# Kernel tuning notes

Hardware: AMD Instinct MI355X
Metric: run time of the kernel (lower is better)

## Reference

```python
import jax, jax.numpy as jnp
import numpy as np

DIM = 192
HEADS = 6
WS = (4, 8, 8)  # window size (D, H, W)
N = WS[0] * WS[1] * WS[2]  # 256 tokens per window
NW = 64
B_ = 256  # batch * nW


def _relative_position_index(ws):
    d, h, w = ws
    coords = jnp.stack(jnp.meshgrid(jnp.arange(d), jnp.arange(h), jnp.arange(w), indexing='ij'))
    coords = coords.reshape(3, -1)  # (3, N)
    rel = coords[:, :, None] - coords[:, None, :]  # (3, N, N)
    rel = rel.transpose(1, 2, 0) + jnp.array([d - 1, h - 1, w - 1])
    idx = rel[..., 0] * ((2 * h - 1) * (2 * w - 1)) + rel[..., 1] * (2 * w - 1) + rel[..., 2]
    return idx.astype(jnp.int32)  # (N, N)


def setup_inputs() -> dict:
    key = jax.random.key(0)
    ks = jax.random.split(key, 7)
    table_rows = (2 * WS[0] - 1) * (2 * WS[1] - 1) * (2 * WS[2] - 1)  # 1575
    return {
        'x': jax.random.normal(ks[0], (B_, N, DIM), dtype=jnp.float32),
        'mask': jax.random.normal(ks[1], (NW, N, N), dtype=jnp.float32),
        'qkv_w': jax.random.normal(ks[2], (DIM, 3 * DIM), dtype=jnp.float32) * 0.02,
        'qkv_b': jnp.zeros((3 * DIM,), dtype=jnp.float32),
        'proj_w': jax.random.normal(ks[3], (DIM, DIM), dtype=jnp.float32) * 0.02,
        'proj_b': jnp.zeros((DIM,), dtype=jnp.float32),
        'bias_table': jax.random.normal(ks[4], (table_rows, HEADS), dtype=jnp.float32) * 0.02,
        'rel_index': _relative_position_index(WS),
    }


def reference(x, mask, qkv_w, qkv_b, proj_w, proj_b, bias_table, rel_index):
    B, Ntok, C = x.shape
    hd = C // HEADS
    scale = hd ** (-0.5)
    qkv = (x @ qkv_w + qkv_b).reshape(B, Ntok, 3, HEADS, hd)
    qkv = qkv.transpose(2, 0, 3, 1, 4)  # (3, B, H, N, hd)
    q, k, v = qkv[0], qkv[1], qkv[2]
    attn = jnp.einsum('bhnd,bhmd->bhnm', q * scale, k)  # (B, H, N, N)
    # gathered relative-position bias: (N, N, H) -> (H, N, N)
    bias = bias_table[rel_index.reshape(-1)].reshape(Ntok, Ntok, HEADS).transpose(2, 0, 1)
    attn = attn + bias[None]
    nW = mask.shape[0]
    attn = attn.reshape(B // nW, nW, HEADS, Ntok, Ntok) + mask[None, :, None]
    attn = attn.reshape(B, HEADS, Ntok, Ntok)
    attn = jax.nn.softmax(attn, axis=-1)
    out = jnp.einsum('bhnm,bhmd->bhnd', attn, v)  # (B, H, N, hd)
    out = out.transpose(0, 2, 1, 3).reshape(B, Ntok, C)
    out = out @ proj_w + proj_b
    return out
```

## Files before the change

kernel.cpp:

```cpp
#include <hip/hip_runtime.h>
#include <cstdint>
#include <math.h>

#define DIMC 192
#define NTOK 256
#define HEADS 6
#define HD 32
#define L2E 1.4426950408889634f

typedef __bf16 bf16x8 __attribute__((ext_vector_type(8)));
typedef __bf16 bf16x4 __attribute__((ext_vector_type(4)));
typedef float f32x4 __attribute__((ext_vector_type(4)));

__device__ __forceinline__ void gload_lds16(const __bf16* g, __bf16* l) {
    __builtin_amdgcn_global_load_lds((const __attribute__((address_space(1))) void*)g,
                                     (__attribute__((address_space(3))) void*)l, 16, 0, 0);
}

__global__ void prep(const float* __restrict__ x, __bf16* __restrict__ xb,
                     const float* __restrict__ qkv_w, __bf16* __restrict__ wqt,
                     const float* __restrict__ proj_w, __bf16* __restrict__ wpt,
                     const float* __restrict__ table, const int* __restrict__ rel,
                     __bf16* __restrict__ biasb) {
    const int bid = blockIdx.x, t = threadIdx.x;
    if (bid < 6144) {
        int i = bid * 256 + t;
        float4 a = ((const float4*)x)[i * 2];
        float4 b = ((const float4*)x)[i * 2 + 1];
        bf16x8 o = {(__bf16)a.x, (__bf16)a.y, (__bf16)a.z, (__bf16)a.w,
                    (__bf16)b.x, (__bf16)b.y, (__bf16)b.z, (__bf16)b.w};
        ((bf16x8*)xb)[i] = o;
    } else if (bid < 6576) {
        int i = (bid - 6144) * 256 + t;
        int n = i / DIMC, k = i - n * DIMC;
        wqt[i] = (__bf16)qkv_w[(size_t)k * 576 + n];
    } else if (bid < 6720) {
        int i = (bid - 6576) * 256 + t;
        int n = i / DIMC, k = i - n * DIMC;
        wpt[i] = (__bf16)proj_w[(size_t)k * DIMC + n];
    } else {
        int i = (bid - 6720) * 256 + t;
        int h = i >> 16;
        int r = i & 65535;
        biasb[i] = (__bf16)(table[rel[r] * 6 + h] * L2E);
    }
}

__launch_bounds__(256, 2)
__global__ void qkvbm(const __bf16* __restrict__ A, const __bf16* __restrict__ Wt,
                      const float* __restrict__ bias,
                      __bf16* __restrict__ qo, __bf16* __restrict__ ko, __bf16* __restrict__ vo,
                      const float* __restrict__ mask, const __bf16* __restrict__ biasb,
                      __bf16* __restrict__ bm) {
    __shared__ __bf16 As[256 * 64];
    __shared__ __bf16 Bs[96 * 64];
    const int t = threadIdx.x;
    const int lin = blockIdx.x;

    if (lin >= 1536) {
        int i = (lin - 1536) * 256 + t;
        int w = i >> 13, oct = i & 8191;
        float4 m0 = ((const float4*)mask)[(size_t)w * 16384 + oct * 2];
        float4 m1 = ((const float4*)mask)[(size_t)w * 16384 + oct * 2 + 1];
        #pragma unroll
        for (int h = 0; h < 6; ++h) {
            bf16x8 bb = ((const bf16x8*)biasb)[h * 8192 + oct];
            bf16x8 o = {(__bf16)(m0.x * L2E + (float)bb[0]), (__bf16)(m0.y * L2E + (float)bb[1]),
                        (__bf16)(m0.z * L2E + (float)bb[2]), (__bf16)(m0.w * L2E + (float)bb[3]),
                        (__bf16)(m1.x * L2E + (float)bb[4]), (__bf16)(m1.y * L2E + (float)bb[5]),
                        (__bf16)(m1.z * L2E + (float)bb[6]), (__bf16)(m1.w * L2E + (float)bb[7])};
            ((bf16x8*)bm)[(size_t)(w * 6 + h) * 8192 + oct] = o;
        }
        return;
    }

    const int wv = t >> 6, lane = t & 63;
    const int l16 = lane & 15, quad = lane >> 4;
    const int xcd = lin & 7, pos = lin >> 3;
    const int bx = pos % 6;
    const int by = xcd + (pos / 6) * 8;
    const int m0 = by * 256;
    const int j0 = bx * 96;

    f32x4 acc[4][6];
    #pragma unroll
    for (int mt = 0; mt < 4; ++mt)
        #pragma unroll
        for (int nt = 0; nt < 6; ++nt)
            acc[mt][nt] = (f32x4){0.f, 0.f, 0.f, 0.f};

    for (int kit = 0; kit < 3; ++kit) {
        const int k0 = kit * 64;
        #pragma unroll
        for (int gi = 0; gi < 8; ++gi) {
            int g = wv * 8 + gi;
            int cid = g * 64 + lane;
            int row = cid >> 3, kcs = cid & 7;
            int kcg = kcs ^ (row & 7);
            gload_lds16(A + (size_t)(m0 + row) * DIMC + k0 + kcg * 8, As + g * 512);
        }
        #pragma unroll
        for (int gi = 0; gi < 3; ++gi) {
            int g = wv * 3 + gi;
            int cid = g * 64 + lane;
            int n = cid >> 3, kcs = cid & 7;
            int kcg = kcs ^ (n & 7);
            gload_lds16(Wt + (size_t)(j0 + n) * DIMC + k0 + kcg * 8, Bs + g * 512);
        }
        __syncthreads();
        #pragma unroll
        for (int kk = 0; kk < 2; ++kk) {
            bf16x8 af[4], bfr[6];
            #pragma unroll
            for (int mt = 0; mt < 4; ++mt) {
                int row = wv * 64 + mt * 16 + l16;
                int ch = (kk * 4 + quad) ^ (row & 7);
                af[mt] = *(const bf16x8*)(As + row * 64 + ch * 8);
            }
            #pragma unroll
            for (int nt = 0; nt < 6; ++nt) {
                int n = nt * 16 + l16;
                int ch = (kk * 4 + quad) ^ (n & 7);
                bfr[nt] = *(const bf16x8*)(Bs + n * 64 + ch * 8);
            }
            #pragma unroll
            for (int mt = 0; mt < 4; ++mt)
                #pragma unroll
                for (int nt = 0; nt < 6; ++nt)
                    acc[mt][nt] = __builtin_amdgcn_mfma_f32_16x16x32_bf16(af[mt], bfr[nt], acc[mt][nt], 0, 0, 0);
        }
        __syncthreads();
    }

    const int which = bx >> 1;
    __bf16* outp = which == 0 ? qo : (which == 1 ? ko : vo);
    const float sc = which == 0 ? (0.17677669529663687f * L2E) : 1.0f;
    float bq[6];
    #pragma unroll
    for (int nt = 0; nt < 6; ++nt) bq[nt] = bias[j0 + nt * 16 + l16];
    const int cloc = (bx & 1) * 96;
    const int b = m0 >> 8;

    if (which != 2) {
        __bf16* tile = As + wv * 4096;
        const int TP = 104;
        #pragma unroll
        for (int mt = 0; mt < 4; ++mt) {
            #pragma unroll
            for (int nt = 0; nt < 6; ++nt)
                #pragma unroll
                for (int r = 0; r < 4; ++r)
                    tile[(quad * 4 + r) * TP + nt * 16 + l16] = (__bf16)((acc[mt][nt][r] + bq[nt]) * sc);
            int row = lane >> 2;
            #pragma unroll
            for (int it = 0; it < 3; ++it) {
                int c8 = (lane & 3) + it * 4;
                bf16x8 val = *(const bf16x8*)(tile + row * TP + c8 * 8);
                int n = wv * 64 + mt * 16 + row;
                int cw = cloc + c8 * 8;
                int h = cw >> 5, d0 = cw & 31;
                *(bf16x8*)(outp + (((size_t)b * HEADS + h) * NTOK + n) * HD + d0) = val;
            }
        }
    } else {
        __bf16* tileT = As + wv * 4096;
        #pragma unroll
        for (int mt = 0; mt < 4; ++mt) {
            #pragma unroll
            for (int nt = 0; nt < 6; ++nt)
                #pragma unroll
                for (int r = 0; r < 4; ++r)
                    tileT[(nt * 16 + l16) * 16 + quad * 4 + r] = (__bf16)(acc[mt][nt][r] + bq[nt]);
            int n0 = wv * 64 + mt * 16;
            #pragma unroll
            for (int it = 0; it < 3; ++it) {
                int qid = lane + 64 * it;
                int col = qid >> 1, half = qid & 1;
                bf16x8 val = *(const bf16x8*)(tileT + col * 16 + half * 8);
                int cw = cloc + col;
                int h = cw >> 5, d = cw & 31;
                *(bf16x8*)(outp + (((size_t)b * HEADS + h) * HD + d) * NTOK + n0 + half * 8) = val;
            }
        }
    }
}

__launch_bounds__(256, 4)
__global__ void attn_mfma(const __bf16* __restrict__ qg, const __bf16* __restrict__ kg,
                          const __bf16* __restrict__ vtg, const __bf16* __restrict__ bm,
                          __bf16* __restrict__ aout) {
    __shared__ __bf16 Ks[NTOK * 32];
    __shared__ __bf16 VTs[HD * 256];
    __shared__ __bf16 Ps[4][16][40];

    const int lin = blockIdx.x;
    const int xcd = lin & 7, pos = lin >> 3;
    const int g = xcd + (pos >> 2) * 8;
    const int i4 = pos & 3;
    const int h = g % 6, w = g / 6;
    const int b = i4 * 64 + w;
    const int bh = b * HEADS + h;

    const int t = threadIdx.x;
    const int wv = t >> 6, lane = t & 63;
    const int l16 = lane & 15, quad = lane >> 4;
    const int q0 = wv * 64;
    const size_t base = (size_t)bh * (NTOK * HD);

    #pragma unroll
    for (int it = 0; it < 4; ++it) {
        int grp = it * 4 + wv;
        int cid = grp * 64 + lane;
        int row = cid >> 2, cc = cid & 3;
        int scc = cc ^ ((row >> 1) & 3);
        gload_lds16(kg + base + row * HD + scc * 8, Ks + grp * 512);
    }
    #pragma unroll
    for (int it = 0; it < 4; ++it) {
        int grp = it * 4 + wv;
        int cid = grp * 64 + lane;
        int row = cid >> 5, cc = cid & 31;
        int scc = cc ^ (row & 7);
        gload_lds16(vtg + base + row * NTOK + scc * 8, VTs + grp * 512);
    }
    __syncthreads();

    bf16x8 qf[4];
    #pragma unroll
    for (int qt = 0; qt < 4; ++qt)
        qf[qt] = *(const bf16x8*)(qg + base + (size_t)(q0 + qt * 16 + l16) * HD + quad * 8);

    f32x4 o[4][2];
    #pragma unroll
    for (int qt = 0; qt < 4; ++qt)
        #pragma unroll
        for (int dt = 0; dt < 2; ++dt)
            o[qt][dt] = (f32x4){0.f, 0.f, 0.f, 0.f};
    float rsum[4] = {};

    const __bf16* bmq = bm + (size_t)(w * 6 + h) * 65536 + (size_t)(q0 + l16) * 256 + quad * 4;
    const int ck = quad ^ ((l16 >> 1) & 3);
    const int xv = l16 & 7;

    bf16x4 bmv[4][2];
    #pragma unroll
    for (int qt = 0; qt < 4; ++qt)
        #pragma unroll
        for (int kt = 0; kt < 2; ++kt)
            bmv[qt][kt] = *(const bf16x4*)(bmq + qt * 4096 + kt * 16);

    for (int c = 0; c < 8; ++c) {
        const int kb = c * 32;
        bf16x4 bmn[4][2];
        if (c < 7) {
            #pragma unroll
            for (int qt = 0; qt < 4; ++qt)
                #pragma unroll
                for (int kt = 0; kt < 2; ++kt)
                    bmn[qt][kt] = *(const bf16x4*)(bmq + qt * 4096 + kb + 32 + kt * 16);
        }
        bf16x8 kf[2];
        #pragma unroll
        for (int kt = 0; kt < 2; ++kt)
            kf[kt] = *(const bf16x8*)(Ks + (kb + kt * 16 + l16) * 32 + ck * 8);
        bf16x8 vf[2];
        #pragma unroll
        for (int dt = 0; dt < 2; ++dt) {
            int cv = (c * 4 + quad) ^ xv;
            vf[dt] = *(const bf16x8*)(VTs + (dt * 16 + l16) * 256 + cv * 8);
        }

        #pragma unroll
        for (int qt = 0; qt < 4; ++qt) {
            #pragma unroll
            for (int kt = 0; kt < 2; ++kt) {
                f32x4 s = (f32x4){0.f, 0.f, 0.f, 0.f};
                s = __builtin_amdgcn_mfma_f32_16x16x32_bf16(kf[kt], qf[qt], s, 0, 0, 0);
                bf16x4 pk;
                #pragma unroll
                for (int r = 0; r < 4; ++r) {
                    float p = __builtin_amdgcn_exp2f(s[r] + (float)bmv[qt][kt][r]);
                    rsum[qt] += p;
                    pk[r] = (__bf16)p;
                }
                *(bf16x4*)(&Ps[wv][l16][kt * 16 + quad * 4]) = pk;
            }
            bf16x8 pf = *(const bf16x8*)(&Ps[wv][l16][quad * 8]);
            #pragma unroll
            for (int dt = 0; dt < 2; ++dt)
                o[qt][dt] = __builtin_amdgcn_mfma_f32_16x16x32_bf16(pf, vf[dt], o[qt][dt], 0, 0, 0);
        }
        if (c < 7) {
            #pragma unroll
            for (int qt = 0; qt < 4; ++qt)
                #pragma unroll
                for (int kt = 0; kt < 2; ++kt)
                    bmv[qt][kt] = bmn[qt][kt];
        }
    }

    float rstot[4];
    #pragma unroll
    for (int qt = 0; qt < 4; ++qt) {
        float s = rsum[qt];
        s += __shfl_xor(s, 16);
        s += __shfl_xor(s, 32);
        rstot[qt] = 1.0f / s;
    }
    #pragma unroll
    for (int qt = 0; qt < 4; ++qt) {
        #pragma unroll
        for (int r = 0; r < 4; ++r) {
            float inv = __shfl(rstot[qt], (lane & 48) | (quad * 4 + r));
            int qrow = q0 + qt * 16 + quad * 4 + r;
            #pragma unroll
            for (int dt = 0; dt < 2; ++dt)
                aout[((size_t)b * NTOK + qrow) * DIMC + h * HD + dt * 16 + l16] =
                    (__bf16)(o[qt][dt][r] * inv);
        }
    }
}

__launch_bounds__(256, 2)
__global__ void proj_mfma(const __bf16* __restrict__ A, const __bf16* __restrict__ Wt,
                          const float* __restrict__ bias, float* __restrict__ out) {
    __shared__ __bf16 As[256 * 64];
    __shared__ __bf16 Bs[96 * 64];
    const int t = threadIdx.x;
    const int wv = t >> 6, lane = t & 63;
    const int l16 = lane & 15, quad = lane >> 4;

    const int lin = blockIdx.x + blockIdx.y * 2;
    const int xcd = lin & 7, pos = lin >> 3;
    const int bx = pos & 1;
    const int by = xcd + (pos >> 1) * 8;

    const int m0 = by * 256;
    const int j0 = bx * 96;

    f32x4 acc[4][6];
    #pragma unroll
    for (int mt = 0; mt < 4; ++mt)
        #pragma unroll
        for (int nt = 0; nt < 6; ++nt)
            acc[mt][nt] = (f32x4){0.f, 0.f, 0.f, 0.f};

    for (int kit = 0; kit < 3; ++kit) {
        const int k0 = kit * 64;
        #pragma unroll
        for (int gi = 0; gi < 8; ++gi) {
            int g = wv * 8 + gi;
            int cid = g * 64 + lane;
            int row = cid >> 3, kcs = cid & 7;
            int kcg = kcs ^ (row & 7);
            gload_lds16(A + (size_t)(m0 + row) * DIMC + k0 + kcg * 8, As + g * 512);
        }
        #pragma unroll
        for (int gi = 0; gi < 3; ++gi) {
            int g = wv * 3 + gi;
            int cid = g * 64 + lane;
            int n = cid >> 3, kcs = cid & 7;
            int kcg = kcs ^ (n & 7);
            gload_lds16(Wt + (size_t)(j0 + n) * DIMC + k0 + kcg * 8, Bs + g * 512);
        }
        __syncthreads();
        #pragma unroll
        for (int kk = 0; kk < 2; ++kk) {
            bf16x8 af[4], bfr[6];
            #pragma unroll
            for (int mt = 0; mt < 4; ++mt) {
                int row = wv * 64 + mt * 16 + l16;
                int ch = (kk * 4 + quad) ^ (row & 7);
                af[mt] = *(const bf16x8*)(As + row * 64 + ch * 8);
            }
            #pragma unroll
            for (int nt = 0; nt < 6; ++nt) {
                int n = nt * 16 + l16;
                int ch = (kk * 4 + quad) ^ (n & 7);
                bfr[nt] = *(const bf16x8*)(Bs + n * 64 + ch * 8);
            }
            #pragma unroll
            for (int mt = 0; mt < 4; ++mt)
                #pragma unroll
                for (int nt = 0; nt < 6; ++nt)
                    acc[mt][nt] = __builtin_amdgcn_mfma_f32_16x16x32_bf16(af[mt], bfr[nt], acc[mt][nt], 0, 0, 0);
        }
        __syncthreads();
    }

    #pragma unroll
    for (int nt = 0; nt < 6; ++nt) {
        int colg = j0 + nt * 16 + l16;
        float bv = bias[colg];
        #pragma unroll
        for (int mt = 0; mt < 4; ++mt)
            #pragma unroll
            for (int r = 0; r < 4; ++r) {
                int token = m0 + wv * 64 + mt * 16 + quad * 4 + r;
                out[(size_t)token * DIMC + colg] = acc[mt][nt][r] + bv;
            }
    }
}

extern "C" void kernel_launch(void* const* d_in, const int* in_sizes, int n_in,
                              void* d_out, int out_size, void* d_ws, size_t ws_size,
                              hipStream_t stream) {
    const float* x          = (const float*)d_in[0];
    const float* mask       = (const float*)d_in[1];
    const float* qkv_w      = (const float*)d_in[2];
    const float* qkv_b      = (const float*)d_in[3];
    const float* proj_w     = (const float*)d_in[4];
    const float* proj_b     = (const float*)d_in[5];
    const float* bias_table = (const float*)d_in[6];
    const int*   rel_index  = (const int*)d_in[7];

    char* ws = (char*)d_ws;
    __bf16* xb    = (__bf16*)(ws);
    __bf16* q     = (__bf16*)(ws + 25165824);
    __bf16* k     = (__bf16*)(ws + 50331648);
    __bf16* vT    = (__bf16*)(ws + 75497472);
    __bf16* biasb = (__bf16*)(ws + 100663296);
    __bf16* wqt   = (__bf16*)(ws + 102236160);
    __bf16* wpt   = (__bf16*)(ws + 102457344);
    __bf16* aoutb = xb;
    __bf16* bm    = (__bf16*)d_out;

    prep<<<8256, 256, 0, stream>>>(x, xb, qkv_w, wqt, proj_w, wpt, bias_table, rel_index, biasb);
    qkvbm<<<3584, 256, 0, stream>>>(xb, wqt, qkv_b, q, k, vT, mask, biasb, bm);
    attn_mfma<<<1536, 256, 0, stream>>>(q, k, vT, bm, aoutb);
    proj_mfma<<<dim3(2, 256), 256, 0, stream>>>(aoutb, wpt, proj_b, (float*)d_out);
}
```

Measured before the change: 226.3 us.

## Permute key order so softmax probabilities feed PV MFMA directly from registers

Reorders which key rows each lane loads into the QK^T MFMA so the output accumulator layout matches the A-operand layout of the PV MFMA. This removes the per-wave LDS staging buffer for P, along with its store, reload and implicit synchronization. The bias/mask loads become single 8-wide loads, and the K swizzle is adjusted to the new access pattern. Launch bounds are raised to allow 5 blocks per CU, which may increase register pressure or spills.

```diff
diff --git a/kernel.cpp b/kernel.cpp
--- a/kernel.cpp
+++ b/kernel.cpp
@@ -185,13 +185,12 @@
     }
 }
 
-__launch_bounds__(256, 4)
+__launch_bounds__(256, 5)
 __global__ void attn_mfma(const __bf16* __restrict__ qg, const __bf16* __restrict__ kg,
                           const __bf16* __restrict__ vtg, const __bf16* __restrict__ bm,
                           __bf16* __restrict__ aout) {
     __shared__ __bf16 Ks[NTOK * 32];
     __shared__ __bf16 VTs[HD * 256];
-    __shared__ __bf16 Ps[4][16][40];
 
     const int lin = blockIdx.x;
     const int xcd = lin & 7, pos = lin >> 3;
@@ -212,7 +211,7 @@
         int grp = it * 4 + wv;
         int cid = grp * 64 + lane;
         int row = cid >> 2, cc = cid & 3;
-        int scc = cc ^ ((row >> 1) & 3);
+        int scc = cc ^ (((row >> 1) & 1) | (((row >> 3) & 1) << 1));
         gload_lds16(kg + base + row * HD + scc * 8, Ks + grp * 512);
     }
     #pragma unroll
@@ -238,31 +237,28 @@
             o[qt][dt] = (f32x4){0.f, 0.f, 0.f, 0.f};
     float rsum[4] = {};
 
-    const __bf16* bmq = bm + (size_t)(w * 6 + h) * 65536 + (size_t)(q0 + l16) * 256 + quad * 4;
-    const int ck = quad ^ ((l16 >> 1) & 3);
+    const __bf16* bmq = bm + (size_t)(w * 6 + h) * 65536 + (size_t)(q0 + l16) * 256 + quad * 8;
+    const int kapb = 8 * (l16 >> 2) + (l16 & 3);
+    const int ck = quad ^ ((l16 >> 1) & 1) ^ (((l16 >> 2) & 1) << 1);
     const int xv = l16 & 7;
 
-    bf16x4 bmv[4][2];
+    bf16x8 bmv[4];
     #pragma unroll
     for (int qt = 0; qt < 4; ++qt)
-        #pragma unroll
-        for (int kt = 0; kt < 2; ++kt)
-            bmv[qt][kt] = *(const bf16x4*)(bmq + qt * 4096 + kt * 16);
+        bmv[qt] = *(const bf16x8*)(bmq + qt * 4096);
 
     for (int c = 0; c < 8; ++c) {
         const int kb = c * 32;
-        bf16x4 bmn[4][2];
+        bf16x8 bmn[4];
         if (c < 7) {
             #pragma unroll
             for (int qt = 0; qt < 4; ++qt)
-                #pragma unroll
-                for (int kt = 0; kt < 2; ++kt)
-                    bmn[qt][kt] = *(const bf16x4*)(bmq + qt * 4096 + kb + 32 + kt * 16);
+                bmn[qt] = *(const bf16x8*)(bmq + qt * 4096 + kb + 32);
         }
         bf16x8 kf[2];
         #pragma unroll
         for (int kt = 0; kt < 2; ++kt)
-            kf[kt] = *(const bf16x8*)(Ks + (kb + kt * 16 + l16) * 32 + ck * 8);
+            kf[kt] = *(const bf16x8*)(Ks + (kb + kapb + 4 * kt) * 32 + ck * 8);
         bf16x8 vf[2];
         #pragma unroll
         for (int dt = 0; dt < 2; ++dt) {
@@ -272,20 +268,18 @@
 
         #pragma unroll
         for (int qt = 0; qt < 4; ++qt) {
+            bf16x8 pf;
             #pragma unroll
             for (int kt = 0; kt < 2; ++kt) {
                 f32x4 s = (f32x4){0.f, 0.f, 0.f, 0.f};
                 s = __builtin_amdgcn_mfma_f32_16x16x32_bf16(kf[kt], qf[qt], s, 0, 0, 0);
-                bf16x4 pk;
                 #pragma unroll
                 for (int r = 0; r < 4; ++r) {
-                    float p = __builtin_amdgcn_exp2f(s[r] + (float)bmv[qt][kt][r]);
+                    float p = __builtin_amdgcn_exp2f(s[r] + (float)bmv[qt][kt * 4 + r]);
                     rsum[qt] += p;
-                    pk[r] = (__bf16)p;
+                    pf[kt * 4 + r] = (__bf16)p;
                 }
-                *(bf16x4*)(&Ps[wv][l16][kt * 16 + quad * 4]) = pk;
-            }
-            bf16x8 pf = *(const bf16x8*)(&Ps[wv][l16][quad * 8]);
+            }
             #pragma unroll
             for (int dt = 0; dt < 2; ++dt)
                 o[qt][dt] = __builtin_amdgcn_mfma_f32_16x16x32_bf16(pf, vf[dt], o[qt][dt], 0, 0, 0);
@@ -293,9 +287,7 @@
         if (c < 7) {
             #pragma unroll
             for (int qt = 0; qt < 4; ++qt)
-                #pragma unroll
-                for (int kt = 0; kt < 2; ++kt)
-                    bmv[qt][kt] = bmn[qt][kt];
+                bmv[qt] = bmn[qt];
         }
     }
 
```

Result: slower. 462.8 us (+104.5%).
